# Performance work log

Measured on AMD Instinct MI355X. Metric: run time of the kernel, lower is better.

## Reference

```python
import jax, jax.numpy as jnp
import numpy as np

T1 = 0.001
T2 = 0.5
ALPHA = 1.0
EPS = 1e-6


def setup_inputs() -> dict:
    key = jax.random.key(0)
    k1, k2, k3, k4, k5 = jax.random.split(key, 5)
    N, D, C, P = 1024, 1024, 32768, 128
    x = jax.random.normal(k1, (N, D), dtype=jnp.float32)
    # params.weight init: uniform(-0.05, 0.05); bias filled with 0 in torch, use small randn to exercise grads
    W = jax.random.uniform(k2, (C, D), dtype=jnp.float32, minval=-0.05, maxval=0.05)
    b = jax.random.normal(k3, (C,), dtype=jnp.float32) * 0.01
    rp = jax.random.normal(k4, (D + 1, P), dtype=jnp.float32)  # SimHash random projection (D+1, K*L)
    sample_ids = jax.random.randint(k5, (C,), 0, C, dtype=jnp.int64)  # LSH candidate set
    return {"x": x, "W": W, "b": b, "rp": rp, "sample_ids": sample_ids}


def reference(x, W, b, rp, sample_ids):
    N, D = x.shape
    C = W.shape[0]
    S = sample_ids.shape[0]
    # query_tolsh = cat(x, ones)
    q = jnp.concatenate([x, jnp.ones((N, 1), x.dtype)], axis=1)  # (N, D+1)
    # sparse embedding gather of candidate weights/bias
    sw = W[sample_ids]          # (S, D)
    sb = b[sample_ids]          # (S,)
    sample_product = x @ sw.T   # (N, S)
    sample_logits = sample_product + sb[None, :]
    # kthvalue-based thresholds (torch.kthvalue is 1-indexed, k-th smallest along last dim)
    t1_th = int(C * (1.0 - T1))
    t2_th = int(C * (1.0 - T2))
    sorted_prod = jnp.sort(sample_product, axis=-1)
    t1_ip = jnp.maximum(jnp.mean(sorted_prod[:, t1_th - 1]), 0.0)
    t2_ip = jnp.mean(sorted_prod[:, t2_th - 1])
    pos_mask = sample_product > t1_ip
    neg_mask = sample_product < t2_ip
    # triplet loss on hash-projected cosine similarity; p_x/p_weight/n_x/n_weight are detached in torch
    qd = jax.lax.stop_gradient(q)
    wcat = jax.lax.stop_gradient(jnp.concatenate([sw, sb[:, None]], axis=1))  # (S, D+1)
    qp = qd @ rp    # (N, P)
    wp = wcat @ rp  # (S, P)
    qn = qp / jnp.maximum(jnp.linalg.norm(qp, axis=-1, keepdims=True), EPS)
    wn = wp / jnp.maximum(jnp.linalg.norm(wp, axis=-1, keepdims=True), EPS)
    sim = qn @ wn.T  # (N, S) cosine similarity for every (query, candidate) pair
    # deterministic surrogate for the random-pairing hinge: masked mean sims
    pf = pos_mask.astype(sim.dtype)
    nf = neg_mask.astype(sim.dtype)
    sim_p = jnp.sum(sim * pf) / jnp.maximum(jnp.sum(pf), 1.0)
    sim_n = jnp.sum(sim * nf) / jnp.maximum(jnp.sum(nf), 1.0)
    triplet_loss = jnp.maximum(sim_n - sim_p + ALPHA, 0.0)
    return sample_logits, triplet_loss
```

## Files before the change

kernel.cpp:

```cpp
#include <hip/hip_runtime.h>


using short8v = __attribute__((ext_vector_type(8))) short;
using f32x4   = __attribute__((ext_vector_type(4))) float;

#define AS1C(p) ((const __attribute__((address_space(1))) void*)(p))
#define AS3(p)  ((__attribute__((address_space(3))) void*)(p))

__device__ __forceinline__ unsigned short f2bf(float f) {
  union { float f; unsigned u; } v; v.f = f;
  unsigned u = v.u;
  return (unsigned short)((u + 0x7FFFu + ((u >> 16) & 1u)) >> 16);
}
__device__ __forceinline__ float bf2f(unsigned short s) {
  return __uint_as_float(((unsigned)s) << 16);
}

__global__ __launch_bounds__(256) void k_gather(
    const float* __restrict__ W, const float* __restrict__ bb,
    const float* __restrict__ x, const int* __restrict__ ids,
    unsigned short* __restrict__ swb, float* __restrict__ sbg,
    unsigned short* __restrict__ xb, float* __restrict__ scal,
    const float* __restrict__ rp, unsigned short* __restrict__ qnb) {
  const int t = threadIdx.x;
  if (blockIdx.x >= 2048) {
    __shared__ float xs[4][1024];
    __shared__ float part[4][2];
    const int r0 = (blockIdx.x - 2048) * 4;
#pragma unroll
    for (int i = 0; i < 4; ++i) {
      int idx = i * 256 + t, rr = idx >> 8, c4 = idx & 255;
      *(float4*)&xs[rr][c4 * 4] = *(const float4*)&x[(size_t)(r0 + rr) * 1024 + c4 * 4];
    }
    __syncthreads();
    const int col = t & 127, rsel = t >> 7;
    float a0 = 0.f, a1 = 0.f;
    for (int k = 0; k < 1024; k += 4) {
      float4 xa = *(const float4*)&xs[rsel][k];
      float4 xbv = *(const float4*)&xs[rsel + 2][k];
      float av[4] = {xa.x, xa.y, xa.z, xa.w};
      float bv[4] = {xbv.x, xbv.y, xbv.z, xbv.w};
#pragma unroll
      for (int j = 0; j < 4; ++j) {
        float rv = rp[(size_t)(k + j) * 128 + col];
        a0 += av[j] * rv;
        a1 += bv[j] * rv;
      }
    }
    { float rv = rp[(size_t)1024 * 128 + col]; a0 += rv; a1 += rv; }
    float s0 = a0 * a0, s1 = a1 * a1;
#pragma unroll
    for (int m = 1; m < 64; m <<= 1) { s0 += __shfl_xor(s0, m, 64); s1 += __shfl_xor(s1, m, 64); }
    if ((t & 63) == 0) { part[t >> 6][0] = s0; part[t >> 6][1] = s1; }
    __syncthreads();
    float n0 = part[2 * rsel][0] + part[2 * rsel + 1][0];
    float n1 = part[2 * rsel][1] + part[2 * rsel + 1][1];
    qnb[(size_t)(r0 + rsel) * 128 + col]     = f2bf(a0 / fmaxf(sqrtf(n0), 1e-6f));
    qnb[(size_t)(r0 + rsel + 2) * 128 + col] = f2bf(a1 / fmaxf(sqrtf(n1), 1e-6f));
    return;
  }
  if (blockIdx.x == 0 && t < 6) scal[t] = 0.f;
  for (int blk = blockIdx.x; blk < 33792; blk += 2048) {
    if (blk < 32768) {
      const int id = ids[blk];
      float4 v = *(const float4*)&W[(size_t)id * 1024 + t * 4];
      ushort4 o; o.x = f2bf(v.x); o.y = f2bf(v.y); o.z = f2bf(v.z); o.w = f2bf(v.w);
      *(ushort4*)&swb[(size_t)blk * 1024 + t * 4] = o;
      if (t == 0) sbg[blk] = bb[id];
    } else {
      const int r = blk - 32768;
      float4 v = *(const float4*)&x[(size_t)r * 1024 + t * 4];
      ushort4 o; o.x = f2bf(v.x); o.y = f2bf(v.y); o.z = f2bf(v.z); o.w = f2bf(v.w);
      *(ushort4*)&xb[(size_t)r * 1024 + t * 4] = o;
    }
  }
}

__device__ __forceinline__ void stage_sw(const unsigned short* g, int lda,
                                         unsigned short* l, int t) {
#pragma unroll
  for (int i = 0; i < 2; ++i) {
    const int idx = i * 256 + t;
    const int row = idx >> 2;
    const int c = (idx & 3) ^ ((row >> 1) & 3);
    const unsigned short* gp = g + (size_t)row * lda + c * 8;
    __builtin_amdgcn_global_load_lds(AS1C(gp), AS3(l + idx * 8), 16, 0, 0);
  }
}

__device__ __forceinline__ void stage_rp(const float* __restrict__ rp, int k0,
                                         unsigned short* l, int t) {
#pragma unroll
  for (int ii = 0; ii < 4; ++ii) {
    int idx = ii * 256 + t;
    int kk = idx & 31, c4 = idx >> 5;
    float4 v = *(const float4*)&rp[(size_t)(k0 + kk) * 128 + c4 * 4];
    l[(c4 * 4 + 0) * 32 + kk] = f2bf(v.x);
    l[(c4 * 4 + 1) * 32 + kk] = f2bf(v.y);
    l[(c4 * 4 + 2) * 32 + kk] = f2bf(v.z);
    l[(c4 * 4 + 3) * 32 + kk] = f2bf(v.w);
  }
}

__global__ __launch_bounds__(256) void k_wn(
    const unsigned short* __restrict__ swb, const float* __restrict__ rp,
    const float* __restrict__ sbg, unsigned short* __restrict__ wnb) {
  __shared__ unsigned short As[2][128 * 32];
  __shared__ unsigned short Bs[2][128 * 32];
  __shared__ float nbuf[2][128];
  const int t = threadIdx.x;
  const int r0 = blockIdx.x * 128;
  const unsigned short* Ag = swb + (size_t)r0 * 1024;
  f32x4 acc[4][4];
#pragma unroll
  for (int m = 0; m < 4; ++m)
#pragma unroll
    for (int n = 0; n < 4; ++n) acc[m][n] = f32x4{0.f, 0.f, 0.f, 0.f};
  stage_sw(Ag, 1024, &As[0][0], t);
  stage_rp(rp, 0, &Bs[0][0], t);
  const int l = t & 63, w = t >> 6, wm = w >> 1, wn = w & 1;
  const int lr = l & 15, lk = l >> 4;
  const int kch = lk * 8;
  const int ach = (lk ^ ((lr >> 1) & 3)) * 8;
  for (int kt = 0; kt < 32; ++kt) {
    const int cur = kt & 1;
    __syncthreads();
    if (kt + 1 < 32) {
      stage_sw(Ag + (kt + 1) * 32, 1024, &As[cur ^ 1][0], t);
      stage_rp(rp, (kt + 1) * 32, &Bs[cur ^ 1][0], t);
    }
    short8v a[4], b[4];
#pragma unroll
    for (int m = 0; m < 4; ++m) a[m] = *(const short8v*)&As[cur][(wm * 64 + m * 16 + lr) * 32 + ach];
#pragma unroll
    for (int n = 0; n < 4; ++n) b[n] = *(const short8v*)&Bs[cur][(wn * 64 + n * 16 + lr) * 32 + kch];
#pragma unroll
    for (int m = 0; m < 4; ++m)
#pragma unroll
      for (int n = 0; n < 4; ++n)
        acc[m][n] = __builtin_amdgcn_mfma_f32_16x16x32_bf16(a[m], b[n], acc[m][n], 0, 0, 0);
  }
  const float* rpl = rp + (size_t)1024 * 128;
  float sb_r[4][4];
#pragma unroll
  for (int m = 0; m < 4; ++m)
#pragma unroll
    for (int i = 0; i < 4; ++i)
      sb_r[m][i] = sbg[r0 + wm * 64 + m * 16 + lk * 4 + i];
#pragma unroll
  for (int n = 0; n < 4; ++n) {
    const int gc = wn * 64 + n * 16 + lr;
    const float rl = rpl[gc];
#pragma unroll
    for (int m = 0; m < 4; ++m)
#pragma unroll
      for (int i = 0; i < 4; ++i) acc[m][n][i] += sb_r[m][i] * rl;
  }
#pragma unroll
  for (int m = 0; m < 4; ++m)
#pragma unroll
    for (int i = 0; i < 4; ++i) {
      float s = 0.f;
#pragma unroll
      for (int n = 0; n < 4; ++n) s += acc[m][n][i] * acc[m][n][i];
#pragma unroll
      for (int msk = 1; msk < 16; msk <<= 1) s += __shfl_xor(s, msk, 64);
      if (lr == 0) nbuf[wn][wm * 64 + m * 16 + lk * 4 + i] = s;
    }
  __syncthreads();
#pragma unroll
  for (int m = 0; m < 4; ++m)
#pragma unroll
    for (int i = 0; i < 4; ++i) {
      const int lrow = wm * 64 + m * 16 + lk * 4 + i;
      const float n2 = nbuf[0][lrow] + nbuf[1][lrow];
      const float sc = 1.f / fmaxf(sqrtf(n2), 1e-6f);
#pragma unroll
      for (int n = 0; n < 4; ++n) {
        const int gc = wn * 64 + n * 16 + lr;
        wnb[(size_t)(r0 + lrow) * 128 + gc] = f2bf(acc[m][n][i] * sc);
      }
    }
}

__global__ __launch_bounds__(256) void k_gemm_main(
    const unsigned short* __restrict__ A, const unsigned short* __restrict__ B,
    const float* __restrict__ sbg, float* __restrict__ out) {
  __shared__ unsigned short As[2][128 * 32];
  __shared__ unsigned short Bs[2][128 * 32];
  const int t = threadIdx.x;
  const int lb = (blockIdx.x & 7) * 256 + (blockIdx.x >> 3);
  const int bm = lb & 7, bn = lb >> 3;
  const unsigned short* Ag = A + (size_t)bm * 128 * 1024;
  const unsigned short* Bg = B + (size_t)bn * 128 * 1024;
  f32x4 acc[2][8];
#pragma unroll
  for (int m = 0; m < 2; ++m)
#pragma unroll
    for (int n = 0; n < 8; ++n) acc[m][n] = f32x4{0.f, 0.f, 0.f, 0.f};
  stage_sw(Ag, 1024, &As[0][0], t);
  stage_sw(Bg, 1024, &Bs[0][0], t);
  const int l = t & 63, w = t >> 6;
  const int lr = l & 15, lk = l >> 4;
  const int ach = (lk ^ ((lr >> 1) & 3)) * 8;
  for (int kt = 0; kt < 32; ++kt) {
    const int cur = kt & 1;
    __syncthreads();
    if (kt + 1 < 32) {
      stage_sw(Ag + (kt + 1) * 32, 1024, &As[cur ^ 1][0], t);
      stage_sw(Bg + (kt + 1) * 32, 1024, &Bs[cur ^ 1][0], t);
    }
    short8v a[2], b[8];
#pragma unroll
    for (int m = 0; m < 2; ++m)
      a[m] = *(const short8v*)&As[cur][(w * 32 + m * 16 + lr) * 32 + ach];
#pragma unroll
    for (int n = 0; n < 8; ++n)
      b[n] = *(const short8v*)&Bs[cur][(n * 16 + lr) * 32 + ach];
#pragma unroll
    for (int m = 0; m < 2; ++m)
#pragma unroll
      for (int n = 0; n < 8; ++n)
        acc[m][n] = __builtin_amdgcn_mfma_f32_16x16x32_bf16(a[m], b[n], acc[m][n], 0, 0, 0);
  }
  const int rb = bm * 128 + w * 32, cb = bn * 128;
#pragma unroll
  for (int n = 0; n < 8; ++n) {
    const int gc = cb + n * 16 + lr;
    const float bias = sbg[gc];
#pragma unroll
    for (int m = 0; m < 2; ++m)
#pragma unroll
      for (int i = 0; i < 4; ++i) {
        const int gr = rb + m * 16 + lk * 4 + i;
        out[(size_t)gr * 32768 + gc] = acc[m][n][i] + bias;
      }
  }
}

__global__ __launch_bounds__(1024) void k_hist(
    const float* __restrict__ logits, const float* __restrict__ sbg,
    float* __restrict__ scal) {
  __shared__ unsigned short rowm[32768];
  __shared__ unsigned hist[2048];
  __shared__ unsigned scanbuf[1024];
  __shared__ unsigned hsub[64];
  __shared__ int res[4];
  const int t = threadIdx.x, row = blockIdx.x;
  for (int i = t; i < 2048; i += 1024) hist[i] = 0u;
  if (t < 64) hsub[t] = 0u;
  __syncthreads();
  const float* lp = logits + (size_t)row * 32768;
  for (int c = t * 4; c < 32768; c += 4096) {
    const float4 lv = *(const float4*)&lp[c];
    const float4 sb4 = *(const float4*)&sbg[c];
    const float pr[4] = {lv.x - sb4.x, lv.y - sb4.y, lv.z - sb4.z, lv.w - sb4.w};
    unsigned short mm[4];
#pragma unroll
    for (int j = 0; j < 4; ++j) {
      const unsigned short bbf = f2bf(pr[j]);
      const unsigned m = (bbf & 0x8000u) ? (0xFFFFu ^ (unsigned)bbf)
                                         : ((unsigned)bbf | 0x8000u);
      mm[j] = (unsigned short)m;
      atomicAdd(&hist[m >> 5], 1u);
    }
    *(ushort4*)&rowm[c] = make_ushort4(mm[0], mm[1], mm[2], mm[3]);
  }
  __syncthreads();
  {
    unsigned s = hist[t * 2] + hist[t * 2 + 1];
    scanbuf[t] = s;
    __syncthreads();
    unsigned x = s;
    for (int off = 1; off < 1024; off <<= 1) {
      unsigned y = (t >= off) ? scanbuf[t - off] : 0u;
      __syncthreads();
      x += y; scanbuf[t] = x;
      __syncthreads();
    }
    unsigned run = x - s;
    const unsigned K1R = 32734u, K2R = 16383u;
#pragma unroll
    for (int j = 0; j < 2; ++j) {
      unsigned c = hist[t * 2 + j];
      if (K1R >= run && K1R < run + c) { res[0] = t * 2 + j; res[1] = (int)(K1R - run); }
      if (K2R >= run && K2R < run + c) { res[2] = t * 2 + j; res[3] = (int)(K2R - run); }
      run += c;
    }
  }
  __syncthreads();
  const unsigned bin1 = (unsigned)res[0], r1 = (unsigned)res[1];
  const unsigned bin2 = (unsigned)res[2], r2 = (unsigned)res[3];
  for (int c = t; c < 32768; c += 1024) {
    const unsigned m = rowm[c];
    const unsigned bq = m >> 5;
    if (bq == bin1) atomicAdd(&hsub[m & 31], 1u);
    if (bq == bin2) atomicAdd(&hsub[32 + (m & 31)], 1u);
  }
  __syncthreads();
  if (t == 0) {
    unsigned a_ = 0; int sub1 = 31;
    for (int j = 0; j < 32; ++j) { if (r1 < a_ + hsub[j]) { sub1 = j; break; } a_ += hsub[j]; }
    a_ = 0; int sub2 = 31;
    for (int j = 0; j < 32; ++j) { if (r2 < a_ + hsub[32 + j]) { sub2 = j; break; } a_ += hsub[32 + j]; }
    const unsigned m1 = (bin1 << 5) | (unsigned)sub1;
    const unsigned m2 = (bin2 << 5) | (unsigned)sub2;
    const float kv1 = bf2f((unsigned short)((m1 & 0x8000u) ? (m1 & 0x7FFFu) : (0xFFFFu ^ m1)));
    const float kv2 = bf2f((unsigned short)((m2 & 0x8000u) ? (m2 & 0x7FFFu) : (0xFFFFu ^ m2)));
    atomicAdd(&scal[0], kv1);
    atomicAdd(&scal[1], kv2);
  }
}

__global__ __launch_bounds__(256) void k_sim(
    const unsigned short* __restrict__ A, const unsigned short* __restrict__ B,
    const float* __restrict__ logits, const float* __restrict__ sbg,
    const float* __restrict__ scal, float4* __restrict__ part) {
  __shared__ unsigned short smem[128 * 128];
  __shared__ float red[4][4];
  unsigned short* As = smem;
  unsigned short* Bs = smem + 128 * 32;
  unsigned short* simb = smem;
  const int t = threadIdx.x;
  const int bm = blockIdx.x & 7, bn = blockIdx.x >> 3;
  const unsigned short* Ag = A + (size_t)bm * 128 * 128;
  const unsigned short* Bg = B + (size_t)bn * 128 * 128;
  f32x4 acc[4][4];
#pragma unroll
  for (int m = 0; m < 4; ++m)
#pragma unroll
    for (int n = 0; n < 4; ++n) acc[m][n] = f32x4{0.f, 0.f, 0.f, 0.f};
  const int l = t & 63, w = t >> 6, wm = w >> 1, wn = w & 1;
  const int lr = l & 15, lk = l >> 4;
  const int ach = (lk ^ ((lr >> 1) & 3)) * 8;
  for (int kt = 0; kt < 4; ++kt) {
    stage_sw(Ag + kt * 32, 128, As, t);
    stage_sw(Bg + kt * 32, 128, Bs, t);
    __syncthreads();
    short8v a[4], b[4];
#pragma unroll
    for (int m = 0; m < 4; ++m) a[m] = *(const short8v*)&As[(wm * 64 + m * 16 + lr) * 32 + ach];
#pragma unroll
    for (int n = 0; n < 4; ++n) b[n] = *(const short8v*)&Bs[(wn * 64 + n * 16 + lr) * 32 + ach];
#pragma unroll
    for (int m = 0; m < 4; ++m)
#pragma unroll
      for (int n = 0; n < 4; ++n)
        acc[m][n] = __builtin_amdgcn_mfma_f32_16x16x32_bf16(a[m], b[n], acc[m][n], 0, 0, 0);
    __syncthreads();
  }
#pragma unroll
  for (int m = 0; m < 4; ++m)
#pragma unroll
    for (int n = 0; n < 4; ++n) {
      const int col = wn * 64 + n * 16 + lr;
#pragma unroll
      for (int i = 0; i < 4; ++i) {
        const int row = wm * 64 + m * 16 + lk * 4 + i;
        simb[row * 128 + col] = f2bf(acc[m][n][i]);
      }
    }
  __syncthreads();
  const float t1 = fmaxf(scal[0] * (1.f / 1024.f), 0.f);
  const float t2 = scal[1] * (1.f / 1024.f);
  const int rb0 = bm * 128, cb0 = bn * 128;
  float ps = 0.f, pc = 0.f, ns = 0.f, nc = 0.f;
#pragma unroll
  for (int it = 0; it < 16; ++it) {
    const int idx = it * 256 + t;
    const int rr = idx >> 5;
    const int c4 = idx & 31;
    const float4 lv = *(const float4*)&logits[(size_t)(rb0 + rr) * 32768 + cb0 + c4 * 4];
    const float4 sb4 = *(const float4*)&sbg[cb0 + c4 * 4];
    const ushort4 sv = *(const ushort4*)&simb[rr * 128 + c4 * 4];
    const float pr[4] = {lv.x - sb4.x, lv.y - sb4.y, lv.z - sb4.z, lv.w - sb4.w};
    const float sm[4] = {bf2f(sv.x), bf2f(sv.y), bf2f(sv.z), bf2f(sv.w)};
#pragma unroll
    for (int j = 0; j < 4; ++j) {
      if (pr[j] > t1) { ps += sm[j]; pc += 1.f; }
      if (pr[j] < t2) { ns += sm[j]; nc += 1.f; }
    }
  }
#pragma unroll
  for (int m = 1; m < 64; m <<= 1) {
    ps += __shfl_xor(ps, m, 64); pc += __shfl_xor(pc, m, 64);
    ns += __shfl_xor(ns, m, 64); nc += __shfl_xor(nc, m, 64);
  }
  if (l == 0) { red[w][0] = ps; red[w][1] = pc; red[w][2] = ns; red[w][3] = nc; }
  __syncthreads();
  if (t == 0) {
    float4 o;
    o.x = red[0][0] + red[1][0] + red[2][0] + red[3][0];
    o.y = red[0][1] + red[1][1] + red[2][1] + red[3][1];
    o.z = red[0][2] + red[1][2] + red[2][2] + red[3][2];
    o.w = red[0][3] + red[1][3] + red[2][3] + red[3][3];
    part[blockIdx.x] = o;
  }
}

__global__ __launch_bounds__(256) void k_final(
    const float4* __restrict__ part, float* __restrict__ out) {
  __shared__ float red[4][4];
  const int t = threadIdx.x;
  float ps = 0.f, pc = 0.f, ns = 0.f, nc = 0.f;
  for (int i = t; i < 2048; i += 256) {
    float4 v = part[i];
    ps += v.x; pc += v.y; ns += v.z; nc += v.w;
  }
#pragma unroll
  for (int m = 1; m < 64; m <<= 1) {
    ps += __shfl_xor(ps, m, 64); pc += __shfl_xor(pc, m, 64);
    ns += __shfl_xor(ns, m, 64); nc += __shfl_xor(nc, m, 64);
  }
  const int w = t >> 6;
  if ((t & 63) == 0) { red[w][0] = ps; red[w][1] = pc; red[w][2] = ns; red[w][3] = nc; }
  __syncthreads();
  if (t == 0) {
    float tps = red[0][0] + red[1][0] + red[2][0] + red[3][0];
    float tpc = red[0][1] + red[1][1] + red[2][1] + red[3][1];
    float tns = red[0][2] + red[1][2] + red[2][2] + red[3][2];
    float tnc = red[0][3] + red[1][3] + red[2][3] + red[3][3];
    float sp = tps / fmaxf(tpc, 1.f);
    float sn = tns / fmaxf(tnc, 1.f);
    out[33554432] = fmaxf(sn - sp + 1.f, 0.f);
  }
}

extern "C" void kernel_launch(void* const* d_in, const int* in_sizes, int n_in,
                              void* d_out, int out_size, void* d_ws, size_t ws_size,
                              hipStream_t stream) {
  const float* x  = (const float*)d_in[0];
  const float* W  = (const float*)d_in[1];
  const float* b  = (const float*)d_in[2];
  const float* rp = (const float*)d_in[3];
  const int*  ids = (const int*)d_in[4];
  float* out = (float*)d_out;
  char* ws = (char*)d_ws;

  unsigned short* swb = (unsigned short*)(ws);
  unsigned short* xb  = (unsigned short*)(ws + 67108864);
  float*          sbg = (float*)(ws + 69206016);
  unsigned short* qnb = (unsigned short*)(ws + 69337088);
  unsigned short* wnb = (unsigned short*)(ws + 69599232);
  float*         scal = (float*)(ws + 78012416);
  float4*        part = (float4*)(ws + 78016512);

  k_gather   <<<2304,  256, 0, stream>>>(W, b, x, ids, swb, sbg, xb, scal, rp, qnb);
  k_wn       <<<256,   256, 0, stream>>>(swb, rp, sbg, wnb);
  k_gemm_main<<<2048,  256, 0, stream>>>(xb, swb, sbg, out);
  k_hist     <<<1024, 1024, 0, stream>>>(out, sbg, scal);
  k_sim      <<<2048,  256, 0, stream>>>(qnb, wnb, out, sbg, scal, part);
  k_final    <<<1,     256, 0, stream>>>(part, out);
}
```

Measured before the change: 297.0 us.

## Merge wn projection into main GEMM launch and fold final reduction into k_sim

The separate k_wn kernel is merged into the main logits GEMM as 256 extra blocks of one launch, so the weight-projection work runs alongside the large GEMM instead of in its own launch. The k_final reduction kernel is removed: k_sim blocks atomically accumulate their partial sums into scratch scalars, and the last block, found with an atomic counter, computes the triplet loss. This cuts two kernel launches and the tail of the small wn grid, at the cost of float atomics, which make the summation order nondeterministic, and a last-block pattern that depends on correct fences.

```diff
diff --git a/kernel.cpp b/kernel.cpp
--- a/kernel.cpp
+++ b/kernel.cpp
@@ -59,7 +59,7 @@
     qnb[(size_t)(r0 + rsel + 2) * 128 + col] = f2bf(a1 / fmaxf(sqrtf(n1), 1e-6f));
     return;
   }
-  if (blockIdx.x == 0 && t < 6) scal[t] = 0.f;
+  if (blockIdx.x == 0 && t < 8) scal[t] = 0.f;
   for (int blk = blockIdx.x; blk < 33792; blk += 2048) {
     if (blk < 32768) {
       const int id = ids[blk];
@@ -102,93 +102,91 @@
   }
 }
 
-__global__ __launch_bounds__(256) void k_wn(
-    const unsigned short* __restrict__ swb, const float* __restrict__ rp,
-    const float* __restrict__ sbg, unsigned short* __restrict__ wnb) {
-  __shared__ unsigned short As[2][128 * 32];
-  __shared__ unsigned short Bs[2][128 * 32];
+__global__ __launch_bounds__(256) void k_gemm_wn(
+    const unsigned short* __restrict__ A, const unsigned short* __restrict__ B,
+    const float* __restrict__ sbg, float* __restrict__ out,
+    const float* __restrict__ rp, unsigned short* __restrict__ wnb) {
+  __shared__ unsigned short AsU[2][128 * 32];
+  __shared__ unsigned short BsU[2][128 * 32];
   __shared__ float nbuf[2][128];
   const int t = threadIdx.x;
-  const int r0 = blockIdx.x * 128;
-  const unsigned short* Ag = swb + (size_t)r0 * 1024;
-  f32x4 acc[4][4];
-#pragma unroll
-  for (int m = 0; m < 4; ++m)
-#pragma unroll
-    for (int n = 0; n < 4; ++n) acc[m][n] = f32x4{0.f, 0.f, 0.f, 0.f};
-  stage_sw(Ag, 1024, &As[0][0], t);
-  stage_rp(rp, 0, &Bs[0][0], t);
-  const int l = t & 63, w = t >> 6, wm = w >> 1, wn = w & 1;
+  const int l = t & 63, w = t >> 6;
   const int lr = l & 15, lk = l >> 4;
-  const int kch = lk * 8;
   const int ach = (lk ^ ((lr >> 1) & 3)) * 8;
-  for (int kt = 0; kt < 32; ++kt) {
-    const int cur = kt & 1;
-    __syncthreads();
-    if (kt + 1 < 32) {
-      stage_sw(Ag + (kt + 1) * 32, 1024, &As[cur ^ 1][0], t);
-      stage_rp(rp, (kt + 1) * 32, &Bs[cur ^ 1][0], t);
-    }
-    short8v a[4], b[4];
-#pragma unroll
-    for (int m = 0; m < 4; ++m) a[m] = *(const short8v*)&As[cur][(wm * 64 + m * 16 + lr) * 32 + ach];
-#pragma unroll
-    for (int n = 0; n < 4; ++n) b[n] = *(const short8v*)&Bs[cur][(wn * 64 + n * 16 + lr) * 32 + kch];
+
+  if (blockIdx.x >= 2048) {
+    const int r0 = (blockIdx.x - 2048) * 128;
+    const unsigned short* Ag = B + (size_t)r0 * 1024;
+    f32x4 acc[4][4];
 #pragma unroll
     for (int m = 0; m < 4; ++m)
 #pragma unroll
-      for (int n = 0; n < 4; ++n)
-        acc[m][n] = __builtin_amdgcn_mfma_f32_16x16x32_bf16(a[m], b[n], acc[m][n], 0, 0, 0);
-  }
-  const float* rpl = rp + (size_t)1024 * 128;
-  float sb_r[4][4];
-#pragma unroll
-  for (int m = 0; m < 4; ++m)
-#pragma unroll
-    for (int i = 0; i < 4; ++i)
-      sb_r[m][i] = sbg[r0 + wm * 64 + m * 16 + lk * 4 + i];
-#pragma unroll
-  for (int n = 0; n < 4; ++n) {
-    const int gc = wn * 64 + n * 16 + lr;
-    const float rl = rpl[gc];
+      for (int n = 0; n < 4; ++n) acc[m][n] = f32x4{0.f, 0.f, 0.f, 0.f};
+    stage_sw(Ag, 1024, &AsU[0][0], t);
+    stage_rp(rp, 0, &BsU[0][0], t);
+    const int wm = w >> 1, wn = w & 1;
+    const int kch = lk * 8;
+    for (int kt = 0; kt < 32; ++kt) {
+      const int cur = kt & 1;
+      __syncthreads();
+      if (kt + 1 < 32) {
+        stage_sw(Ag + (kt + 1) * 32, 1024, &AsU[cur ^ 1][0], t);
+        stage_rp(rp, (kt + 1) * 32, &BsU[cur ^ 1][0], t);
+      }
+      short8v a[4], b[4];
+#pragma unroll
+      for (int m = 0; m < 4; ++m) a[m] = *(const short8v*)&AsU[cur][(wm * 64 + m * 16 + lr) * 32 + ach];
+#pragma unroll
+      for (int n = 0; n < 4; ++n) b[n] = *(const short8v*)&BsU[cur][(wn * 64 + n * 16 + lr) * 32 + kch];
+#pragma unroll
+      for (int m = 0; m < 4; ++m)
+#pragma unroll
+        for (int n = 0; n < 4; ++n)
+          acc[m][n] = __builtin_amdgcn_mfma_f32_16x16x32_bf16(a[m], b[n], acc[m][n], 0, 0, 0);
+    }
+    const float* rpl = rp + (size_t)1024 * 128;
+    float sb_r[4][4];
 #pragma unroll
     for (int m = 0; m < 4; ++m)
 #pragma unroll
-      for (int i = 0; i < 4; ++i) acc[m][n][i] += sb_r[m][i] * rl;
-  }
-#pragma unroll
-  for (int m = 0; m < 4; ++m)
-#pragma unroll
-    for (int i = 0; i < 4; ++i) {
-      float s = 0.f;
-#pragma unroll
-      for (int n = 0; n < 4; ++n) s += acc[m][n][i] * acc[m][n][i];
-#pragma unroll
-      for (int msk = 1; msk < 16; msk <<= 1) s += __shfl_xor(s, msk, 64);
-      if (lr == 0) nbuf[wn][wm * 64 + m * 16 + lk * 4 + i] = s;
-    }
-  __syncthreads();
-#pragma unroll
-  for (int m = 0; m < 4; ++m)
-#pragma unroll
-    for (int i = 0; i < 4; ++i) {
-      const int lrow = wm * 64 + m * 16 + lk * 4 + i;
-      const float n2 = nbuf[0][lrow] + nbuf[1][lrow];
-      const float sc = 1.f / fmaxf(sqrtf(n2), 1e-6f);
-#pragma unroll
-      for (int n = 0; n < 4; ++n) {
-        const int gc = wn * 64 + n * 16 + lr;
-        wnb[(size_t)(r0 + lrow) * 128 + gc] = f2bf(acc[m][n][i] * sc);
-      }
-    }
-}
-
-__global__ __launch_bounds__(256) void k_gemm_main(
-    const unsigned short* __restrict__ A, const unsigned short* __restrict__ B,
-    const float* __restrict__ sbg, float* __restrict__ out) {
-  __shared__ unsigned short As[2][128 * 32];
-  __shared__ unsigned short Bs[2][128 * 32];
-  const int t = threadIdx.x;
+      for (int i = 0; i < 4; ++i)
+        sb_r[m][i] = sbg[r0 + wm * 64 + m * 16 + lk * 4 + i];
+#pragma unroll
+    for (int n = 0; n < 4; ++n) {
+      const int gc = wn * 64 + n * 16 + lr;
+      const float rl = rpl[gc];
+#pragma unroll
+      for (int m = 0; m < 4; ++m)
+#pragma unroll
+        for (int i = 0; i < 4; ++i) acc[m][n][i] += sb_r[m][i] * rl;
+    }
+#pragma unroll
+    for (int m = 0; m < 4; ++m)
+#pragma unroll
+      for (int i = 0; i < 4; ++i) {
+        float s = 0.f;
+#pragma unroll
+        for (int n = 0; n < 4; ++n) s += acc[m][n][i] * acc[m][n][i];
+#pragma unroll
+        for (int msk = 1; msk < 16; msk <<= 1) s += __shfl_xor(s, msk, 64);
+        if (lr == 0) nbuf[wn][wm * 64 + m * 16 + lk * 4 + i] = s;
+      }
+    __syncthreads();
+#pragma unroll
+    for (int m = 0; m < 4; ++m)
+#pragma unroll
+      for (int i = 0; i < 4; ++i) {
+        const int lrow = wm * 64 + m * 16 + lk * 4 + i;
+        const float n2 = nbuf[0][lrow] + nbuf[1][lrow];
+        const float sc = 1.f / fmaxf(sqrtf(n2), 1e-6f);
+#pragma unroll
+        for (int n = 0; n < 4; ++n) {
+          const int gc = wn * 64 + n * 16 + lr;
+          wnb[(size_t)(r0 + lrow) * 128 + gc] = f2bf(acc[m][n][i] * sc);
+        }
+      }
+    return;
+  }
   const int lb = (blockIdx.x & 7) * 256 + (blockIdx.x >> 3);
   const int bm = lb & 7, bn = lb >> 3;
   const unsigned short* Ag = A + (size_t)bm * 128 * 1024;
@@ -198,25 +196,22 @@
   for (int m = 0; m < 2; ++m)
 #pragma unroll
     for (int n = 0; n < 8; ++n) acc[m][n] = f32x4{0.f, 0.f, 0.f, 0.f};
-  stage_sw(Ag, 1024, &As[0][0], t);
-  stage_sw(Bg, 1024, &Bs[0][0], t);
-  const int l = t & 63, w = t >> 6;
-  const int lr = l & 15, lk = l >> 4;
-  const int ach = (lk ^ ((lr >> 1) & 3)) * 8;
+  stage_sw(Ag, 1024, &AsU[0][0], t);
+  stage_sw(Bg, 1024, &BsU[0][0], t);
   for (int kt = 0; kt < 32; ++kt) {
     const int cur = kt & 1;
     __syncthreads();
     if (kt + 1 < 32) {
-      stage_sw(Ag + (kt + 1) * 32, 1024, &As[cur ^ 1][0], t);
-      stage_sw(Bg + (kt + 1) * 32, 1024, &Bs[cur ^ 1][0], t);
+      stage_sw(Ag + (kt + 1) * 32, 1024, &AsU[cur ^ 1][0], t);
+      stage_sw(Bg + (kt + 1) * 32, 1024, &BsU[cur ^ 1][0], t);
     }
     short8v a[2], b[8];
 #pragma unroll
     for (int m = 0; m < 2; ++m)
-      a[m] = *(const short8v*)&As[cur][(w * 32 + m * 16 + lr) * 32 + ach];
+      a[m] = *(const short8v*)&AsU[cur][(w * 32 + m * 16 + lr) * 32 + ach];
 #pragma unroll
     for (int n = 0; n < 8; ++n)
-      b[n] = *(const short8v*)&Bs[cur][(n * 16 + lr) * 32 + ach];
+      b[n] = *(const short8v*)&BsU[cur][(n * 16 + lr) * 32 + ach];
 #pragma unroll
     for (int m = 0; m < 2; ++m)
 #pragma unroll
@@ -315,7 +310,7 @@
 __global__ __launch_bounds__(256) void k_sim(
     const unsigned short* __restrict__ A, const unsigned short* __restrict__ B,
     const float* __restrict__ logits, const float* __restrict__ sbg,
-    const float* __restrict__ scal, float4* __restrict__ part) {
+    float* __restrict__ scal, float* __restrict__ out) {
   __shared__ unsigned short smem[128 * 128];
   __shared__ float red[4][4];
   unsigned short* As = smem;
@@ -389,40 +384,23 @@
   if (l == 0) { red[w][0] = ps; red[w][1] = pc; red[w][2] = ns; red[w][3] = nc; }
   __syncthreads();
   if (t == 0) {
-    float4 o;
-    o.x = red[0][0] + red[1][0] + red[2][0] + red[3][0];
-    o.y = red[0][1] + red[1][1] + red[2][1] + red[3][1];
-    o.z = red[0][2] + red[1][2] + red[2][2] + red[3][2];
-    o.w = red[0][3] + red[1][3] + red[2][3] + red[3][3];
-    part[blockIdx.x] = o;
-  }
-}
-
-__global__ __launch_bounds__(256) void k_final(
-    const float4* __restrict__ part, float* __restrict__ out) {
-  __shared__ float red[4][4];
-  const int t = threadIdx.x;
-  float ps = 0.f, pc = 0.f, ns = 0.f, nc = 0.f;
-  for (int i = t; i < 2048; i += 256) {
-    float4 v = part[i];
-    ps += v.x; pc += v.y; ns += v.z; nc += v.w;
-  }
-#pragma unroll
-  for (int m = 1; m < 64; m <<= 1) {
-    ps += __shfl_xor(ps, m, 64); pc += __shfl_xor(pc, m, 64);
-    ns += __shfl_xor(ns, m, 64); nc += __shfl_xor(nc, m, 64);
-  }
-  const int w = t >> 6;
-  if ((t & 63) == 0) { red[w][0] = ps; red[w][1] = pc; red[w][2] = ns; red[w][3] = nc; }
-  __syncthreads();
-  if (t == 0) {
-    float tps = red[0][0] + red[1][0] + red[2][0] + red[3][0];
-    float tpc = red[0][1] + red[1][1] + red[2][1] + red[3][1];
-    float tns = red[0][2] + red[1][2] + red[2][2] + red[3][2];
-    float tnc = red[0][3] + red[1][3] + red[2][3] + red[3][3];
-    float sp = tps / fmaxf(tpc, 1.f);
-    float sn = tns / fmaxf(tnc, 1.f);
-    out[33554432] = fmaxf(sn - sp + 1.f, 0.f);
+    atomicAdd(&scal[2], red[0][0] + red[1][0] + red[2][0] + red[3][0]);
+    atomicAdd(&scal[3], red[0][1] + red[1][1] + red[2][1] + red[3][1]);
+    atomicAdd(&scal[4], red[0][2] + red[1][2] + red[2][2] + red[3][2]);
+    atomicAdd(&scal[5], red[0][3] + red[1][3] + red[2][3] + red[3][3]);
+    __threadfence();
+    unsigned* cnt = (unsigned*)&scal[6];
+    const unsigned old = atomicAdd(cnt, 1u);
+    if (old == 2047u) {
+      __threadfence();
+      const float tps = atomicAdd(&scal[2], 0.f);
+      const float tpc = atomicAdd(&scal[3], 0.f);
+      const float tns = atomicAdd(&scal[4], 0.f);
+      const float tnc = atomicAdd(&scal[5], 0.f);
+      const float sp = tps / fmaxf(tpc, 1.f);
+      const float sn = tns / fmaxf(tnc, 1.f);
+      out[33554432] = fmaxf(sn - sp + 1.f, 0.f);
+    }
   }
 }
 
@@ -443,12 +421,9 @@
   unsigned short* qnb = (unsigned short*)(ws + 69337088);
   unsigned short* wnb = (unsigned short*)(ws + 69599232);
   float*         scal = (float*)(ws + 78012416);
-  float4*        part = (float4*)(ws + 78016512);
-
-  k_gather   <<<2304,  256, 0, stream>>>(W, b, x, ids, swb, sbg, xb, scal, rp, qnb);
-  k_wn       <<<256,   256, 0, stream>>>(swb, rp, sbg, wnb);
-  k_gemm_main<<<2048,  256, 0, stream>>>(xb, swb, sbg, out);
-  k_hist     <<<1024, 1024, 0, stream>>>(out, sbg, scal);
-  k_sim      <<<2048,  256, 0, stream>>>(qnb, wnb, out, sbg, scal, part);
-  k_final    <<<1,     256, 0, stream>>>(part, out);
-}
+
+  k_gather <<<2304,  256, 0, stream>>>(W, b, x, ids, swb, sbg, xb, scal, rp, qnb);
+  k_gemm_wn<<<2304,  256, 0, stream>>>(xb, swb, sbg, out, rp, wnb);
+  k_hist   <<<1024, 1024, 0, stream>>>(out, sbg, scal);
+  k_sim    <<<2048,  256, 0, stream>>>(qnb, wnb, out, sbg, scal, out);
+}
```

After: 432.3 us. +45.6%, slower.
